# Optimization experiments

Measured on AMD Instinct MI355X. Metric: run time of the kernel, lower is better.

The kernel has to match this reference:

```python
import jax, jax.numpy as jnp
import numpy as np

B, T, D, E = 8, 512, 128, 256

def setup_inputs() -> dict:
    key = jax.random.key(0)
    ks = jax.random.split(key, 6)
    s_d = 1.0 / np.sqrt(D)
    return {
        "x": jax.random.normal(ks[0], (B, T, D), jnp.float32),
        "Wg": jax.random.normal(ks[1], (D, E), jnp.float32) * s_d,
        "bg": jnp.zeros((E,), jnp.float32),
        "expert_w": jax.random.normal(ks[2], (E, D, D), jnp.float32) * s_d,
        "w1": jax.random.normal(ks[3], (D, D), jnp.float32) * s_d,
        "b1": jnp.zeros((D,), jnp.float32),
        "w2": jax.random.normal(ks[4], (D, D), jnp.float32) * s_d,
        "b2": jnp.zeros((D,), jnp.float32),
    }

def reference(x, Wg, bg, expert_w, w1, b1, w2, b2):
    n_experts = expert_w.shape[0]
    # router (context=None -> route on x itself)
    gate_scores = jax.nn.softmax(x @ Wg + bg, axis=-1)            # [B,T,E]
    top_vals, top_idx = jax.lax.top_k(gate_scores, 2)             # [B,T,2]
    top_w = top_vals / (jnp.sum(top_vals, axis=-1, keepdims=True) + 1e-6)
    # dense per-expert projection (faithful to original einsum over ALL experts)
    expert_outputs = jnp.einsum('btd,edo->bteo', x, expert_w)     # [B,T,E,D]
    # top-2 one-hot mask with normalized weights -> [B,T,E]
    mask = jnp.sum(jax.nn.one_hot(top_idx, n_experts, dtype=x.dtype) * top_w[..., None], axis=2)
    mixed = jnp.einsum('bteo,bte->bto', expert_outputs, mask)     # [B,T,D]
    # SwiGLU
    g = mixed @ w1 + b1
    weighted_avg = g * jax.nn.sigmoid(g) * (mixed @ w2 + b2)      # [B,T,D]
    # variance consensus against swiglu output
    diff_sq = jnp.square(expert_outputs - weighted_avg[:, :, None, :])
    weighted_var = jnp.einsum('bteo,bte->bto', diff_sq, mask)     # [B,T,D]
    consensus = jnp.exp(-jnp.mean(weighted_var, axis=-1))         # [B,T]
    return weighted_avg, consensus
```

## Files before the change

### kernel.cpp

```cpp
#include <hip/hip_runtime.h>
#include <math.h>

#define NT  4096
#define DD  128
#define EE  256
#define CAP 2048

__global__ __launch_bounds__(256) void logits_kernel(
    const float* __restrict__ x, const float* __restrict__ Wg,
    const float* __restrict__ bg, float* __restrict__ logits,
    int* __restrict__ cnt)
{
    const int bid = blockIdx.x;
    const int tid = threadIdx.x;
    if (bid == 0) cnt[tid] = 0;

    __shared__ float xt[DD][8];

    {
        const int q = tid >> 5, part = tid & 31;
        const float4 v = *(reinterpret_cast<const float4*>(
            x + (size_t)(bid * 8 + q) * DD) + part);
        xt[part * 4 + 0][q] = v.x;
        xt[part * 4 + 1][q] = v.y;
        xt[part * 4 + 2][q] = v.z;
        xt[part * 4 + 3][q] = v.w;
    }
    __syncthreads();

    const int e = tid;
    const float be = bg[e];
    float a0 = be, a1 = be, a2 = be, a3 = be;
    float a4 = be, a5 = be, a6 = be, a7 = be;
    #pragma unroll 8
    for (int d = 0; d < DD; ++d) {
        const float w = Wg[(size_t)d * EE + e];
        const float4 xa = *reinterpret_cast<const float4*>(&xt[d][0]);
        const float4 xb = *reinterpret_cast<const float4*>(&xt[d][4]);
        a0 = fmaf(xa.x, w, a0);  a1 = fmaf(xa.y, w, a1);
        a2 = fmaf(xa.z, w, a2);  a3 = fmaf(xa.w, w, a3);
        a4 = fmaf(xb.x, w, a4);  a5 = fmaf(xb.y, w, a5);
        a6 = fmaf(xb.z, w, a6);  a7 = fmaf(xb.w, w, a7);
    }
    float* lr = logits + (size_t)(bid * 8) * EE + e;
    lr[0 * EE] = a0;  lr[1 * EE] = a1;  lr[2 * EE] = a2;  lr[3 * EE] = a3;
    lr[4 * EE] = a4;  lr[5 * EE] = a5;  lr[6 * EE] = a6;  lr[7 * EE] = a7;
}

__global__ __launch_bounds__(256) void top2_kernel(
    const float* __restrict__ logits, float2* __restrict__ w_out,
    int* __restrict__ cnt, int* __restrict__ plist)
{
    const int lane = threadIdx.x & 63;
    const int t    = blockIdx.x * 4 + (threadIdx.x >> 6);
    const float4 lg = *reinterpret_cast<const float4*>(logits + (size_t)t * EE + lane * 4);
    float v[4] = {lg.x, lg.y, lg.z, lg.w};

    float m = v[0]; int mi = lane * 4;
    #pragma unroll
    for (int j = 1; j < 4; ++j)
        if (v[j] > m) { m = v[j]; mi = lane * 4 + j; }
    #pragma unroll
    for (int s = 32; s; s >>= 1) {
        const float om = __shfl_xor(m, s);
        const int   oi = __shfl_xor(mi, s);
        if (om > m || (om == m && oi < mi)) { m = om; mi = oi; }
    }

    float ssum = 0.0f;
    #pragma unroll
    for (int j = 0; j < 4; ++j) ssum += __expf(v[j] - m);
    #pragma unroll
    for (int s = 32; s; s >>= 1) ssum += __shfl_xor(ssum, s);

    float m2 = -INFINITY; int mi2 = 0;
    #pragma unroll
    for (int j = 0; j < 4; ++j) {
        const int ei = lane * 4 + j;
        if (ei != mi && v[j] > m2) { m2 = v[j]; mi2 = ei; }
    }
    #pragma unroll
    for (int s = 32; s; s >>= 1) {
        const float om = __shfl_xor(m2, s);
        const int   oi = __shfl_xor(mi2, s);
        if (om > m2 || (om == m2 && oi < mi2)) { m2 = om; mi2 = oi; }
    }

    if (lane == 0) {
        const float p1 = 1.0f / ssum;
        const float p2 = __expf(m2 - m) / ssum;
        const float den = p1 + p2 + 1e-6f;
        w_out[t] = make_float2(p1 / den, p2 / den);
        const int pos1 = atomicAdd(&cnt[mi], 1);
        if (pos1 < CAP) plist[mi * CAP + pos1] = t * 2;
        const int pos2 = atomicAdd(&cnt[mi2], 1);
        if (pos2 < CAP) plist[mi2 * CAP + pos2] = t * 2 + 1;
    }
}

__global__ __launch_bounds__(128) void expert_kernel(
    const float* __restrict__ x, const float* __restrict__ ew,
    const int* __restrict__ cnt, const int* __restrict__ plist,
    float* __restrict__ ybuf)
{
    const int wg = (blockIdx.x & 7) * 256 + (blockIdx.x >> 3);
    const int e  = wg >> 3;
    const int c  = wg & 7;
    int n = cnt[e];
    if (n > CAP) n = CAP;
    if (n <= c) return;

    const int o   = threadIdx.x;
    const int* pl = plist + e * CAP;
    const float* W = ew + (size_t)e * DD * DD;

    __shared__ float xt[DD][8];
    __shared__ int   fis[8];

    for (int base = c; base < n; base += 64) {
        {
            const int q = o >> 4, part = o & 15;
            if (base + q * 8 < n) {
                const int fi = pl[base + q * 8];
                if (part == 0) fis[q] = fi;
                const float4* xr = reinterpret_cast<const float4*>(
                    x + (size_t)(fi >> 1) * DD) + part * 2;
                const float4 u0 = xr[0], u1 = xr[1];
                xt[part * 8 + 0][q] = u0.x;  xt[part * 8 + 1][q] = u0.y;
                xt[part * 8 + 2][q] = u0.z;  xt[part * 8 + 3][q] = u0.w;
                xt[part * 8 + 4][q] = u1.x;  xt[part * 8 + 5][q] = u1.y;
                xt[part * 8 + 6][q] = u1.z;  xt[part * 8 + 7][q] = u1.w;
            }
        }
        __syncthreads();

        float a0 = 0.f, a1 = 0.f, a2 = 0.f, a3 = 0.f;
        float a4 = 0.f, a5 = 0.f, a6 = 0.f, a7 = 0.f;
        #pragma unroll 8
        for (int d = 0; d < DD; ++d) {
            const float w = W[(size_t)d * DD + o];
            const float4 xa = *reinterpret_cast<const float4*>(&xt[d][0]);
            const float4 xb = *reinterpret_cast<const float4*>(&xt[d][4]);
            a0 = fmaf(xa.x, w, a0);  a1 = fmaf(xa.y, w, a1);
            a2 = fmaf(xa.z, w, a2);  a3 = fmaf(xa.w, w, a3);
            a4 = fmaf(xb.x, w, a4);  a5 = fmaf(xb.y, w, a5);
            a6 = fmaf(xb.z, w, a6);  a7 = fmaf(xb.w, w, a7);
        }

        if (base + 0 * 8 < n) ybuf[(size_t)fis[0] * DD + o] = a0;
        if (base + 1 * 8 < n) ybuf[(size_t)fis[1] * DD + o] = a1;
        if (base + 2 * 8 < n) ybuf[(size_t)fis[2] * DD + o] = a2;
        if (base + 3 * 8 < n) ybuf[(size_t)fis[3] * DD + o] = a3;
        if (base + 4 * 8 < n) ybuf[(size_t)fis[4] * DD + o] = a4;
        if (base + 5 * 8 < n) ybuf[(size_t)fis[5] * DD + o] = a5;
        if (base + 6 * 8 < n) ybuf[(size_t)fis[6] * DD + o] = a6;
        if (base + 7 * 8 < n) ybuf[(size_t)fis[7] * DD + o] = a7;
        __syncthreads();
    }
}

__global__ __launch_bounds__(256) void swiglu_kernel(
    const float* __restrict__ ybuf, const float2* __restrict__ ww,
    const float* __restrict__ w1, const float* __restrict__ b1,
    const float* __restrict__ w2, const float* __restrict__ b2,
    float* __restrict__ out_avg, float* __restrict__ out_cons)
{
    const int tid = threadIdx.x;
    const int t0  = blockIdx.x * 8;

    __shared__ float mt[DD][8];
    __shared__ float gh[2][8][DD];

    {
        const int q = tid >> 5, part = tid & 31;
        const int t = t0 + q;
        const float2 w = ww[t];
        const float4 a = *(reinterpret_cast<const float4*>(
            ybuf + (size_t)(2 * t) * DD) + part);
        const float4 b = *(reinterpret_cast<const float4*>(
            ybuf + (size_t)(2 * t + 1) * DD) + part);
        mt[part * 4 + 0][q] = w.x * a.x + w.y * b.x;
        mt[part * 4 + 1][q] = w.x * a.y + w.y * b.y;
        mt[part * 4 + 2][q] = w.x * a.z + w.y * b.z;
        mt[part * 4 + 3][q] = w.x * a.w + w.y * b.w;
    }
    __syncthreads();

    {
        const int o = tid & 127, h = tid >> 7;
        const float* Wc = h ? w2 : w1;
        const float bias = h ? b2[o] : b1[o];
        float a0 = bias, a1 = bias, a2 = bias, a3 = bias;
        float a4 = bias, a5 = bias, a6 = bias, a7 = bias;
        #pragma unroll 8
        for (int d = 0; d < DD; ++d) {
            const float w = Wc[(size_t)d * DD + o];
            const float4 xa = *reinterpret_cast<const float4*>(&mt[d][0]);
            const float4 xb = *reinterpret_cast<const float4*>(&mt[d][4]);
            a0 = fmaf(xa.x, w, a0);  a1 = fmaf(xa.y, w, a1);
            a2 = fmaf(xa.z, w, a2);  a3 = fmaf(xa.w, w, a3);
            a4 = fmaf(xb.x, w, a4);  a5 = fmaf(xb.y, w, a5);
            a6 = fmaf(xb.z, w, a6);  a7 = fmaf(xb.w, w, a7);
        }
        gh[h][0][o] = a0;  gh[h][1][o] = a1;  gh[h][2][o] = a2;  gh[h][3][o] = a3;
        gh[h][4][o] = a4;  gh[h][5][o] = a5;  gh[h][6][o] = a6;  gh[h][7][o] = a7;
    }
    __syncthreads();

    {
        const int q = tid >> 5, part = tid & 31;
        const int t = t0 + q;
        const float2 w = ww[t];
        const float4 a = *(reinterpret_cast<const float4*>(
            ybuf + (size_t)(2 * t) * DD) + part);
        const float4 b = *(reinterpret_cast<const float4*>(
            ybuf + (size_t)(2 * t + 1) * DD) + part);
        const float4 gv = *reinterpret_cast<const float4*>(&gh[0][q][part * 4]);
        const float4 hv = *reinterpret_cast<const float4*>(&gh[1][q][part * 4]);

        float4 r; float v = 0.0f;
        {
            const float g = gv.x, sig = 1.0f / (1.0f + __expf(-g));
            r.x = g * sig * hv.x;
            const float da = a.x - r.x, db = b.x - r.x;
            v += w.x * da * da + w.y * db * db;
        }
        {
            const float g = gv.y, sig = 1.0f / (1.0f + __expf(-g));
            r.y = g * sig * hv.y;
            const float da = a.y - r.y, db = b.y - r.y;
            v += w.x * da * da + w.y * db * db;
        }
        {
            const float g = gv.z, sig = 1.0f / (1.0f + __expf(-g));
            r.z = g * sig * hv.z;
            const float da = a.z - r.z, db = b.z - r.z;
            v += w.x * da * da + w.y * db * db;
        }
        {
            const float g = gv.w, sig = 1.0f / (1.0f + __expf(-g));
            r.w = g * sig * hv.w;
            const float da = a.w - r.w, db = b.w - r.w;
            v += w.x * da * da + w.y * db * db;
        }
        *(reinterpret_cast<float4*>(out_avg + (size_t)t * DD) + part) = r;

        #pragma unroll
        for (int s = 16; s; s >>= 1) v += __shfl_down(v, s);
        if (part == 0) out_cons[t] = __expf(-v * (1.0f / DD));
    }
}

extern "C" void kernel_launch(void* const* d_in, const int* in_sizes, int n_in,
                              void* d_out, int out_size, void* d_ws, size_t ws_size,
                              hipStream_t stream) {
    const float* x   = (const float*)d_in[0];
    const float* Wg  = (const float*)d_in[1];
    const float* bg  = (const float*)d_in[2];
    const float* ew  = (const float*)d_in[3];
    const float* w1  = (const float*)d_in[4];
    const float* b1  = (const float*)d_in[5];
    const float* w2  = (const float*)d_in[6];
    const float* b2  = (const float*)d_in[7];

    float* out_avg  = (float*)d_out;
    float* out_cons = out_avg + (size_t)NT * DD;

    char* ws = (char*)d_ws;
    float*  logits = (float*)ws;
    float*  ybuf   = logits;
    float2* wwp    = (float2*)(ws + 4 * 1024 * 1024);
    int*    cnt    = (int*)   (ws + 4 * 1024 * 1024 + 32 * 1024);
    int*    plist  = (int*)   (ws + 4 * 1024 * 1024 + 64 * 1024);

    logits_kernel<<<NT / 8, 256, 0, stream>>>(x, Wg, bg, logits, cnt);
    top2_kernel  <<<NT / 4, 256, 0, stream>>>(logits, wwp, cnt, plist);
    expert_kernel<<<EE * 8, 128, 0, stream>>>(x, ew, cnt, plist, ybuf);
    swiglu_kernel<<<NT / 8, 256, 0, stream>>>(ybuf, wwp, w1, b1, w2, b2,
                                              out_avg, out_cons);
}
```

Measured before the change: 52.74 us.

## Fuse router logits with top-2 and build per-block expert lists locally

```diff
diff --git a/kernel.cpp b/kernel.cpp
--- a/kernel.cpp
+++ b/kernel.cpp
@@ -4,23 +4,23 @@
 #define NT  4096
 #define DD  128
 #define EE  256
-#define CAP 2048
-
-__global__ __launch_bounds__(256) void logits_kernel(
+
+__global__ __launch_bounds__(256) void router_kernel(
     const float* __restrict__ x, const float* __restrict__ Wg,
-    const float* __restrict__ bg, float* __restrict__ logits,
-    int* __restrict__ cnt)
+    const float* __restrict__ bg, float2* __restrict__ ww,
+    int2* __restrict__ sel)
 {
     const int bid = blockIdx.x;
     const int tid = threadIdx.x;
-    if (bid == 0) cnt[tid] = 0;
+    const int t0  = bid * 8;
 
     __shared__ float xt[DD][8];
+    __shared__ float lg[8][EE];
 
     {
         const int q = tid >> 5, part = tid & 31;
         const float4 v = *(reinterpret_cast<const float4*>(
-            x + (size_t)(bid * 8 + q) * DD) + part);
+            x + (size_t)(t0 + q) * DD) + part);
         xt[part * 4 + 0][q] = v.x;
         xt[part * 4 + 1][q] = v.y;
         xt[part * 4 + 2][q] = v.z;
@@ -28,101 +28,111 @@
     }
     __syncthreads();
 
-    const int e = tid;
-    const float be = bg[e];
-    float a0 = be, a1 = be, a2 = be, a3 = be;
-    float a4 = be, a5 = be, a6 = be, a7 = be;
-    #pragma unroll 8
-    for (int d = 0; d < DD; ++d) {
-        const float w = Wg[(size_t)d * EE + e];
-        const float4 xa = *reinterpret_cast<const float4*>(&xt[d][0]);
-        const float4 xb = *reinterpret_cast<const float4*>(&xt[d][4]);
-        a0 = fmaf(xa.x, w, a0);  a1 = fmaf(xa.y, w, a1);
-        a2 = fmaf(xa.z, w, a2);  a3 = fmaf(xa.w, w, a3);
-        a4 = fmaf(xb.x, w, a4);  a5 = fmaf(xb.y, w, a5);
-        a6 = fmaf(xb.z, w, a6);  a7 = fmaf(xb.w, w, a7);
-    }
-    float* lr = logits + (size_t)(bid * 8) * EE + e;
-    lr[0 * EE] = a0;  lr[1 * EE] = a1;  lr[2 * EE] = a2;  lr[3 * EE] = a3;
-    lr[4 * EE] = a4;  lr[5 * EE] = a5;  lr[6 * EE] = a6;  lr[7 * EE] = a7;
-}
-
-__global__ __launch_bounds__(256) void top2_kernel(
-    const float* __restrict__ logits, float2* __restrict__ w_out,
-    int* __restrict__ cnt, int* __restrict__ plist)
-{
-    const int lane = threadIdx.x & 63;
-    const int t    = blockIdx.x * 4 + (threadIdx.x >> 6);
-    const float4 lg = *reinterpret_cast<const float4*>(logits + (size_t)t * EE + lane * 4);
-    float v[4] = {lg.x, lg.y, lg.z, lg.w};
-
-    float m = v[0]; int mi = lane * 4;
+    {
+        const int e = tid;
+        const float be = bg[e];
+        float a0 = be, a1 = be, a2 = be, a3 = be;
+        float a4 = be, a5 = be, a6 = be, a7 = be;
+        #pragma unroll 8
+        for (int d = 0; d < DD; ++d) {
+            const float w = Wg[(size_t)d * EE + e];
+            const float4 xa = *reinterpret_cast<const float4*>(&xt[d][0]);
+            const float4 xb = *reinterpret_cast<const float4*>(&xt[d][4]);
+            a0 = fmaf(xa.x, w, a0);  a1 = fmaf(xa.y, w, a1);
+            a2 = fmaf(xa.z, w, a2);  a3 = fmaf(xa.w, w, a3);
+            a4 = fmaf(xb.x, w, a4);  a5 = fmaf(xb.y, w, a5);
+            a6 = fmaf(xb.z, w, a6);  a7 = fmaf(xb.w, w, a7);
+        }
+        lg[0][e] = a0;  lg[1][e] = a1;  lg[2][e] = a2;  lg[3][e] = a3;
+        lg[4][e] = a4;  lg[5][e] = a5;  lg[6][e] = a6;  lg[7][e] = a7;
+    }
+    __syncthreads();
+
+    const int lane = tid & 63;
+    const int wv   = tid >> 6;
     #pragma unroll
-    for (int j = 1; j < 4; ++j)
-        if (v[j] > m) { m = v[j]; mi = lane * 4 + j; }
-    #pragma unroll
-    for (int s = 32; s; s >>= 1) {
-        const float om = __shfl_xor(m, s);
-        const int   oi = __shfl_xor(mi, s);
-        if (om > m || (om == m && oi < mi)) { m = om; mi = oi; }
-    }
-
-    float ssum = 0.0f;
-    #pragma unroll
-    for (int j = 0; j < 4; ++j) ssum += __expf(v[j] - m);
-    #pragma unroll
-    for (int s = 32; s; s >>= 1) ssum += __shfl_xor(ssum, s);
-
-    float m2 = -INFINITY; int mi2 = 0;
-    #pragma unroll
-    for (int j = 0; j < 4; ++j) {
-        const int ei = lane * 4 + j;
-        if (ei != mi && v[j] > m2) { m2 = v[j]; mi2 = ei; }
-    }
-    #pragma unroll
-    for (int s = 32; s; s >>= 1) {
-        const float om = __shfl_xor(m2, s);
-        const int   oi = __shfl_xor(mi2, s);
-        if (om > m2 || (om == m2 && oi < mi2)) { m2 = om; mi2 = oi; }
-    }
-
-    if (lane == 0) {
-        const float p1 = 1.0f / ssum;
-        const float p2 = __expf(m2 - m) / ssum;
-        const float den = p1 + p2 + 1e-6f;
-        w_out[t] = make_float2(p1 / den, p2 / den);
-        const int pos1 = atomicAdd(&cnt[mi], 1);
-        if (pos1 < CAP) plist[mi * CAP + pos1] = t * 2;
-        const int pos2 = atomicAdd(&cnt[mi2], 1);
-        if (pos2 < CAP) plist[mi2 * CAP + pos2] = t * 2 + 1;
+    for (int rep = 0; rep < 2; ++rep) {
+        const int tk = wv * 2 + rep;
+        const int t  = t0 + tk;
+        const float4 lv = *reinterpret_cast<const float4*>(&lg[tk][lane * 4]);
+        float v[4] = {lv.x, lv.y, lv.z, lv.w};
+
+        float m = v[0]; int mi = lane * 4;
+        #pragma unroll
+        for (int j = 1; j < 4; ++j)
+            if (v[j] > m) { m = v[j]; mi = lane * 4 + j; }
+        #pragma unroll
+        for (int s = 32; s; s >>= 1) {
+            const float om = __shfl_xor(m, s);
+            const int   oi = __shfl_xor(mi, s);
+            if (om > m || (om == m && oi < mi)) { m = om; mi = oi; }
+        }
+
+        float ssum = 0.0f;
+        #pragma unroll
+        for (int j = 0; j < 4; ++j) ssum += __expf(v[j] - m);
+        #pragma unroll
+        for (int s = 32; s; s >>= 1) ssum += __shfl_xor(ssum, s);
+
+        float m2 = -INFINITY; int mi2 = 0;
+        #pragma unroll
+        for (int j = 0; j < 4; ++j) {
+            const int ei = lane * 4 + j;
+            if (ei != mi && v[j] > m2) { m2 = v[j]; mi2 = ei; }
+        }
+        #pragma unroll
+        for (int s = 32; s; s >>= 1) {
+            const float om = __shfl_xor(m2, s);
+            const int   oi = __shfl_xor(mi2, s);
+            if (om > m2 || (om == m2 && oi < mi2)) { m2 = om; mi2 = oi; }
+        }
+
+        if (lane == 0) {
+            const float p1 = 1.0f / ssum;
+            const float p2 = __expf(m2 - m) / ssum;
+            const float den = p1 + p2 + 1e-6f;
+            ww[t]  = make_float2(p1 / den, p2 / den);
+            sel[t] = make_int2(mi, mi2);
+        }
     }
 }
 
 __global__ __launch_bounds__(128) void expert_kernel(
     const float* __restrict__ x, const float* __restrict__ ew,
-    const int* __restrict__ cnt, const int* __restrict__ plist,
-    float* __restrict__ ybuf)
+    const int2* __restrict__ sel, float* __restrict__ ybuf)
 {
-    const int wg = (blockIdx.x & 7) * 256 + (blockIdx.x >> 3);
-    const int e  = wg >> 3;
-    const int c  = wg & 7;
-    int n = cnt[e];
-    if (n > CAP) n = CAP;
-    if (n <= c) return;
-
-    const int o   = threadIdx.x;
-    const int* pl = plist + e * CAP;
+    const int wg = (blockIdx.x & 7) * 128 + (blockIdx.x >> 3);
+    const int e  = wg >> 2;
+    const int c  = wg & 3;
+    const int tid = threadIdx.x;
+
+    __shared__ float xt[DD][8];
+    __shared__ int   lst[128];
+    __shared__ int   lcnt;
+    if (tid == 0) lcnt = 0;
+    __syncthreads();
+
+    const int tbase = c * 1024;
+    #pragma unroll
+    for (int it = 0; it < 8; ++it) {
+        const int tok = tbase + it * 128 + tid;
+        const int2 s = sel[tok];
+        if (s.x == e) { const int p = atomicAdd(&lcnt, 1); if (p < 128) lst[p] = 2 * tok; }
+        if (s.y == e) { const int p = atomicAdd(&lcnt, 1); if (p < 128) lst[p] = 2 * tok + 1; }
+    }
+    __syncthreads();
+    int n = lcnt;
+    if (n > 128) n = 128;
+    if (n == 0) return;
+
+    const int o = tid;
     const float* W = ew + (size_t)e * DD * DD;
 
-    __shared__ float xt[DD][8];
-    __shared__ int   fis[8];
-
-    for (int base = c; base < n; base += 64) {
-        {
-            const int q = o >> 4, part = o & 15;
-            if (base + q * 8 < n) {
-                const int fi = pl[base + q * 8];
-                if (part == 0) fis[q] = fi;
+    for (int base = 0; base < n; base += 8) {
+        {
+            const int q = tid >> 4, part = tid & 15;
+            if (base + q < n) {
+                const int fi = lst[base + q];
                 const float4* xr = reinterpret_cast<const float4*>(
                     x + (size_t)(fi >> 1) * DD) + part * 2;
                 const float4 u0 = xr[0], u1 = xr[1];
@@ -147,14 +157,14 @@
             a6 = fmaf(xb.z, w, a6);  a7 = fmaf(xb.w, w, a7);
         }
 
-        if (base + 0 * 8 < n) ybuf[(size_t)fis[0] * DD + o] = a0;
-        if (base + 1 * 8 < n) ybuf[(size_t)fis[1] * DD + o] = a1;
-        if (base + 2 * 8 < n) ybuf[(size_t)fis[2] * DD + o] = a2;
-        if (base + 3 * 8 < n) ybuf[(size_t)fis[3] * DD + o] = a3;
-        if (base + 4 * 8 < n) ybuf[(size_t)fis[4] * DD + o] = a4;
-        if (base + 5 * 8 < n) ybuf[(size_t)fis[5] * DD + o] = a5;
-        if (base + 6 * 8 < n) ybuf[(size_t)fis[6] * DD + o] = a6;
-        if (base + 7 * 8 < n) ybuf[(size_t)fis[7] * DD + o] = a7;
+        if (base + 0 < n) ybuf[(size_t)lst[base + 0] * DD + o] = a0;
+        if (base + 1 < n) ybuf[(size_t)lst[base + 1] * DD + o] = a1;
+        if (base + 2 < n) ybuf[(size_t)lst[base + 2] * DD + o] = a2;
+        if (base + 3 < n) ybuf[(size_t)lst[base + 3] * DD + o] = a3;
+        if (base + 4 < n) ybuf[(size_t)lst[base + 4] * DD + o] = a4;
+        if (base + 5 < n) ybuf[(size_t)lst[base + 5] * DD + o] = a5;
+        if (base + 6 < n) ybuf[(size_t)lst[base + 6] * DD + o] = a6;
+        if (base + 7 < n) ybuf[(size_t)lst[base + 7] * DD + o] = a7;
         __syncthreads();
     }
 }
@@ -267,15 +277,12 @@
     float* out_cons = out_avg + (size_t)NT * DD;
 
     char* ws = (char*)d_ws;
-    float*  logits = (float*)ws;
-    float*  ybuf   = logits;
-    float2* wwp    = (float2*)(ws + 4 * 1024 * 1024);
-    int*    cnt    = (int*)   (ws + 4 * 1024 * 1024 + 32 * 1024);
-    int*    plist  = (int*)   (ws + 4 * 1024 * 1024 + 64 * 1024);
-
-    logits_kernel<<<NT / 8, 256, 0, stream>>>(x, Wg, bg, logits, cnt);
-    top2_kernel  <<<NT / 4, 256, 0, stream>>>(logits, wwp, cnt, plist);
-    expert_kernel<<<EE * 8, 128, 0, stream>>>(x, ew, cnt, plist, ybuf);
+    float*  ybuf = (float*)ws;
+    float2* wwp  = (float2*)(ws + 4 * 1024 * 1024);
+    int2*   selp = (int2*)  (ws + 4 * 1024 * 1024 + 32 * 1024);
+
+    router_kernel<<<NT / 8, 256, 0, stream>>>(x, Wg, bg, wwp, selp);
+    expert_kernel<<<EE * 4, 128, 0, stream>>>(x, ew, selp, ybuf);
     swiglu_kernel<<<NT / 8, 256, 0, stream>>>(ybuf, wwp, w1, b1, w2, b2,
                                               out_avg, out_cons);
 }
```

After: 49.61 us. 5.9% less time.
